# Performance work log

Hardware: AMD Instinct MI355X
Metric: run time of the kernel (lower is better)

Reference implementation:

```python
import jax, jax.numpy as jnp
import numpy as np


def _forward(x, wc, we, Wb1, bb1, Wb2, bb2, Wr1, br1, Wr2, br2,
             Wq1, bq1, Wq2, bq2, Wq3, bq3, Wo1, bo1, Wo2, bo2, Wo3, bo3, scale):
    bs, c, h, w = x.shape
    Hs, Ws = scale * h, scale * w
    fh = (jnp.arange(Hs, dtype=jnp.float32) + 0.5) / scale
    fw = (jnp.arange(Ws, dtype=jnp.float32) + 0.5) / scale
    coor_h = fh - jnp.floor(fh + 0.001) - 0.5  # [Hs] fractional phase
    coor_w = fw - jnp.floor(fw + 0.001) - 0.5  # [Ws]
    ones_hw = jnp.ones((Hs, Ws), jnp.float32)
    meta = jnp.stack([ones_hw, ones_hw / scale,
                      jnp.broadcast_to(coor_h[:, None], (Hs, Ws)),
                      jnp.broadcast_to(coor_w[None, :], (Hs, Ws))], 0)  # [4,Hs,Ws]
    chan_mean = x.mean(axis=(0, 2, 3))  # [c]
    chan_scale = jnp.concatenate([chan_mean[:, None], jnp.ones((c, 3), jnp.float32)], axis=1)  # [c,4]
    inp = meta[None] * chan_scale[:, :, None, None]  # [c,4,Hs,Ws]

    # body: 1x1x1 Conv3d over spectral-channel axis c
    lin = lambda W, b, t: jnp.einsum('oc,cfhw->ofhw', W, t) + b[:, None, None, None]
    emb = jax.nn.relu(lin(Wb2, bb2, jax.nn.relu(lin(Wb1, bb1, inp))))  # [c,4,Hs,Ws]

    # offset head: Conv2d 1x1 with batch = c, features = 4 -> 2
    lin2 = lambda W, b, t: jnp.einsum('of,cfhw->cohw', W, t) + b[None, :, None, None]
    off = lin2(Wo3, bo3, jax.nn.relu(lin2(Wo2, bo2, jax.nn.relu(lin2(Wo1, bo1, emb)))))  # [c,2,Hs,Ws]

    # routing_1: Conv3d over c -> 1 channel, sigmoid
    r = jax.nn.sigmoid(lin(Wr2, br2, jax.nn.relu(lin(Wr1, br1, emb))))[0]  # [4,Hs,Ws]
    # routing_2: Conv2d 1x1 over the 4 meta-features -> E experts
    lin3 = lambda W, b, t: jnp.einsum('of,fhw->ohw', W, t) + b[:, None, None]
    rw = jax.nn.sigmoid(lin3(Wq3, bq3, jax.nn.relu(lin3(Wq2, bq2, jax.nn.relu(lin3(Wq1, bq1, r))))))  # [E,Hs,Ws]

    # per-channel offset grid_sample (bilinear, zeros padding, align_corners=True)
    px0 = fw - 0.5  # [Ws] base source x coord
    py0 = fh - 0.5  # [Hs]

    def sample(img, offx, offy):  # img [bs,h,w]; off* [Hs,Ws]
        px = px0[None, :] + offx
        py = py0[:, None] + offy
        x0 = jnp.floor(px); y0 = jnp.floor(py)
        wx = px - x0; wy = py - y0
        x0i = x0.astype(jnp.int32); y0i = y0.astype(jnp.int32)
        def g(yi, xi):
            v = ((xi >= 0) & (xi <= w - 1) & (yi >= 0) & (yi <= h - 1)).astype(img.dtype)
            return img[:, jnp.clip(yi, 0, h - 1), jnp.clip(xi, 0, w - 1)] * v[None]
        return (g(y0i, x0i) * ((1 - wy) * (1 - wx))[None]
                + g(y0i, x0i + 1) * ((1 - wy) * wx)[None]
                + g(y0i + 1, x0i) * (wy * (1 - wx))[None]
                + g(y0i + 1, x0i + 1) * (wy * wx)[None])

    fea0 = jax.vmap(lambda xi, oi: sample(xi, oi[0], oi[1]),
                    in_axes=(1, 0), out_axes=1)(x, off)  # [bs,c,Hs,Ws]

    # per-pixel expert-mixed compress/expand: (sum_e r_e Wc_e) f then (sum_e r_e We_e)
    mid = jnp.einsum('ehw,ekc,bchw->bkhw', rw, wc, fea0)   # [bs,c//8,Hs,Ws]
    out = jnp.einsum('ehw,eck,bkhw->bchw', rw, we, mid)    # [bs,c,Hs,Ws]
    return out + fea0


def setup_inputs() -> dict:
    key = jax.random.key(0)
    ks = jax.random.split(key, 32)
    bs, c, h, w = 4, 64, 64, 64
    E, k = 4, c // 8
    s = 0.05
    d = {
        'x': jax.random.normal(ks[0], (bs, c, h, w), jnp.float32),
        'wc': jax.random.normal(ks[1], (E, k, c), jnp.float32) * s,
        'we': jax.random.normal(ks[2], (E, c, k), jnp.float32) * s,
        'Wb1': jax.random.normal(ks[3], (c, c), jnp.float32) * s,
        'bb1': jax.random.normal(ks[4], (c,), jnp.float32) * s,
        'Wb2': jax.random.normal(ks[5], (c, c), jnp.float32) * s,
        'bb2': jax.random.normal(ks[6], (c,), jnp.float32) * s,
        'Wr1': jax.random.normal(ks[7], (64, c), jnp.float32) * s,
        'br1': jax.random.normal(ks[8], (64,), jnp.float32) * s,
        'Wr2': jax.random.normal(ks[9], (1, 64), jnp.float32) * s,
        'br2': jax.random.normal(ks[10], (1,), jnp.float32) * s,
        'Wq1': jax.random.normal(ks[11], (64, 4), jnp.float32) * s,
        'bq1': jax.random.normal(ks[12], (64,), jnp.float32) * s,
        'Wq2': jax.random.normal(ks[13], (64, 64), jnp.float32) * s,
        'bq2': jax.random.normal(ks[14], (64,), jnp.float32) * s,
        'Wq3': jax.random.normal(ks[15], (E, 64), jnp.float32) * s,
        'bq3': jax.random.normal(ks[16], (E,), jnp.float32) * s,
        'Wo1': jax.random.normal(ks[17], (64, 4), jnp.float32) * s,
        'bo1': jax.random.normal(ks[18], (64,), jnp.float32) * s,
        'Wo2': jax.random.normal(ks[19], (64, 64), jnp.float32) * s,
        'bo2': jax.random.normal(ks[20], (64,), jnp.float32) * s,
        'Wo3': jax.random.normal(ks[21], (2, 64), jnp.float32) * s,
        'bo3': jax.random.normal(ks[22], (2,), jnp.float32) * s,
        'scale': 4,
    }
    return d


def reference(x, wc, we, Wb1, bb1, Wb2, bb2, Wr1, br1, Wr2, br2,
              Wq1, bq1, Wq2, bq2, Wq3, bq3, Wo1, bo1, Wo2, bo2, Wo3, bo3, scale):
    return _forward(x, wc, we, Wb1, bb1, Wb2, bb2, Wr1, br1, Wr2, br2,
                    Wq1, bq1, Wq2, bq2, Wq3, bq3, Wo1, bo1, Wo2, bo2, Wo3, bo3, int(scale))
```

## Files before the change

kernel.cpp:

```cpp
#include <hip/hip_runtime.h>


__device__ __forceinline__ float relu_(float v){ return fmaxf(v, 0.f); }
__device__ __forceinline__ float sigm_(float v){ return 1.f/(1.f + __expf(-v)); }

__global__ void k_mean(const float* __restrict__ x, float* __restrict__ ws) {
  const int ch = blockIdx.x, b = blockIdx.y, t = threadIdx.x;
  const float4* p = reinterpret_cast<const float4*>(x + (size_t)(b*64 + ch)*4096);
  float4 v0 = p[t], v1 = p[t+256], v2 = p[t+512], v3 = p[t+768];
  float s = ((v0.x+v0.y)+(v0.z+v0.w)) + ((v1.x+v1.y)+(v1.z+v1.w))
          + ((v2.x+v2.y)+(v2.z+v2.w)) + ((v3.x+v3.y)+(v3.z+v3.w));
  __shared__ float red[256];
  red[t] = s; __syncthreads();
  for (int off = 128; off > 0; off >>= 1) {
    if (t < off) red[t] += red[t + off];
    __syncthreads();
  }
  if (t == 0) ws[18496 + b*64 + ch] = red[0];
}

__launch_bounds__(256)
__global__ void k_phase(const float* __restrict__ wc, const float* __restrict__ we,
    const float* __restrict__ Wb1, const float* __restrict__ bb1,
    const float* __restrict__ Wb2, const float* __restrict__ bb2,
    const float* __restrict__ Wr1, const float* __restrict__ br1,
    const float* __restrict__ Wr2, const float* __restrict__ br2,
    const float* __restrict__ Wq1, const float* __restrict__ bq1,
    const float* __restrict__ Wq2, const float* __restrict__ bq2,
    const float* __restrict__ Wq3, const float* __restrict__ bq3,
    const float* __restrict__ Wo1, const float* __restrict__ bo1,
    const float* __restrict__ Wo2, const float* __restrict__ bo2,
    const float* __restrict__ Wo3, const float* __restrict__ bo3,
    float* __restrict__ ws)
{
  const int p = blockIdx.x, pi = p >> 2, pj = p & 3;
  const int t = threadIdx.x;
  const float chv = 0.25f*pi - 0.375f, cwv = 0.25f*pj - 0.375f;

  __shared__ float WbL1[64*66];
  __shared__ float WbL2[64*66];
  __shared__ float WrL1[64*66];
  __shared__ float WqL2[64*66];
  __shared__ __align__(16) float Wo2L[4096];
  __shared__ __align__(16) float Wo1L[256];
  __shared__ __align__(16) float wcL[2048];
  __shared__ __align__(16) float weL[2048];
  __shared__ float Wo3L[128];
  __shared__ float Wq1L[256], Wq3L[256];
  __shared__ float Wr2L[64];
  __shared__ float bb1L[64], bb2L[64], br1L[64], bq1L[64], bq2L[64];
  __shared__ float bo1L[64], bo2L[64];

  __shared__ float meanL[64];
  __shared__ __align__(16) float t1L[64][4];
  __shared__ __align__(16) float embL[64][4];
  __shared__ __align__(16) float rpL[64][4];
  __shared__ float r4[4];
  __shared__ float q1L[64], q2L[64];
  __shared__ float rwL[4];
  __shared__ float oxL[64][4], oyL[64][4];

  {
    const float* srcs[4] = {Wb1, Wb2, Wr1, Wq2};
    float* dsts[4] = {WbL1, WbL2, WrL1, WqL2};
    for (int m = 0; m < 4; ++m) {
      const float4* W4 = reinterpret_cast<const float4*>(srcs[m]);
      float* WL = dsts[m];
      for (int v = t; v < 1024; v += 256) {
        float4 d = W4[v];
        const int r = v >> 4, c = (v & 15) << 2;
        float* q = &WL[r*66 + c];
        q[0] = d.x; q[1] = d.y; q[2] = d.z; q[3] = d.w;
      }
    }
    for (int v = t; v < 1024; v += 256)
      reinterpret_cast<float4*>(Wo2L)[v] = reinterpret_cast<const float4*>(Wo2)[v];
    for (int v = t; v < 512; v += 256) {
      reinterpret_cast<float4*>(wcL)[v] = reinterpret_cast<const float4*>(wc)[v];
      reinterpret_cast<float4*>(weL)[v] = reinterpret_cast<const float4*>(we)[v];
    }
    if (t < 64) {
      reinterpret_cast<float4*>(Wo1L)[t] = reinterpret_cast<const float4*>(Wo1)[t];
      reinterpret_cast<float4*>(Wq1L)[t] = reinterpret_cast<const float4*>(Wq1)[t];
      reinterpret_cast<float4*>(Wq3L)[t] = reinterpret_cast<const float4*>(Wq3)[t];
      bb1L[t] = bb1[t]; bb2L[t] = bb2[t]; br1L[t] = br1[t];
      bq1L[t] = bq1[t]; bq2L[t] = bq2[t];
      bo1L[t] = bo1[t]; bo2L[t] = bo2[t];
      Wr2L[t] = Wr2[t];
      const float* wsp = ws + 18496;
      meanL[t] = (wsp[t] + wsp[64+t] + wsp[128+t] + wsp[192+t]) * (1.f/16384.f);
    }
    if (t >= 64 && t < 192) Wo3L[t-64] = Wo3[t-64];
  }
  __syncthreads();

  if (t < 64) {
    float a0 = 0.f, as = 0.f;
    const float* row = &WbL1[t*66];
    #pragma unroll 8
    for (int c = 0; c < 64; ++c) { float w = row[c]; a0 += w*meanL[c]; as += w; }
    float bb = bb1L[t];
    t1L[t][0] = relu_(a0 + bb);
    t1L[t][1] = relu_(0.25f*as + bb);
    t1L[t][2] = relu_(chv*as + bb);
    t1L[t][3] = relu_(cwv*as + bb);
  }
  __syncthreads();
  if (t < 64) {
    float bb = bb2L[t];
    float e0=bb,e1=bb,e2=bb,e3=bb;
    const float* row = &WbL2[t*66];
    #pragma unroll 8
    for (int c = 0; c < 64; ++c) {
      float w = row[c];
      float4 tv = *reinterpret_cast<const float4*>(&t1L[c][0]);
      e0 += w*tv.x; e1 += w*tv.y; e2 += w*tv.z; e3 += w*tv.w;
    }
    embL[t][0]=relu_(e0); embL[t][1]=relu_(e1); embL[t][2]=relu_(e2); embL[t][3]=relu_(e3);
  }
  __syncthreads();
  if (t < 64) {
    float bb = br1L[t];
    float p0=bb,p1=bb,p2=bb,p3=bb;
    const float* row = &WrL1[t*66];
    #pragma unroll 8
    for (int c = 0; c < 64; ++c) {
      float w = row[c];
      float4 ev = *reinterpret_cast<const float4*>(&embL[c][0]);
      p0 += w*ev.x; p1 += w*ev.y; p2 += w*ev.z; p3 += w*ev.w;
    }
    rpL[t][0]=relu_(p0); rpL[t][1]=relu_(p1); rpL[t][2]=relu_(p2); rpL[t][3]=relu_(p3);
  }
  __syncthreads();
  if (t < 4) {
    float acc = br2[0];
    #pragma unroll 8
    for (int c = 0; c < 64; ++c) acc += Wr2L[c]*rpL[c][t];
    r4[t] = sigm_(acc);
  }
  __syncthreads();
  if (t < 64) {
    float acc = bq1L[t];
    #pragma unroll
    for (int f = 0; f < 4; ++f) acc += Wq1L[t*4+f]*r4[f];
    q1L[t] = relu_(acc);
  }
  __syncthreads();
  if (t < 64) {
    float acc = bq2L[t];
    const float* row = &WqL2[t*66];
    #pragma unroll 8
    for (int c = 0; c < 64; ++c) acc += row[c]*q1L[c];
    q2L[t] = relu_(acc);
  }
  __syncthreads();
  if (t < 4) {
    float acc = bq3[t];
    #pragma unroll 8
    for (int c = 0; c < 64; ++c) acc += Wq3L[t*64+c]*q2L[c];
    rwL[t] = sigm_(acc);
  }
  __syncthreads();

  {
    const int ch = t & 63, q = t >> 6;
    const float4 e = *reinterpret_cast<const float4*>(&embL[ch][0]);
    float v1[64];
    #pragma unroll
    for (int o = 0; o < 64; ++o) {
      float4 w = *reinterpret_cast<const float4*>(&Wo1L[o*4]);
      v1[o] = relu_(w.x*e.x + w.y*e.y + w.z*e.z + w.w*e.w + bo1L[o]);
    }
    float ox = 0.f, oy = 0.f;
    for (int o = q*16; o < q*16+16; ++o) {
      float acc = bo2L[o];
      const float4* row = reinterpret_cast<const float4*>(&Wo2L[o*64]);
      #pragma unroll
      for (int k = 0; k < 16; ++k) {
        float4 w = row[k];
        acc += w.x*v1[4*k+0] + w.y*v1[4*k+1] + w.z*v1[4*k+2] + w.w*v1[4*k+3];
      }
      acc = relu_(acc);
      ox += Wo3L[o]*acc;
      oy += Wo3L[64+o]*acc;
    }
    oxL[ch][q] = ox; oyL[ch][q] = oy;
  }
  __syncthreads();

  float* ws_off = ws + 64;
  float* ws_wcT = ws + 2112;
  float* ws_weT = ws + 10304;
  if (t < 64) {
    ws_off[(p*64+t)*2+0] = oxL[t][0]+oxL[t][1]+oxL[t][2]+oxL[t][3] + bo3[0];
    ws_off[(p*64+t)*2+1] = oyL[t][0]+oyL[t][1]+oyL[t][2]+oyL[t][3] + bo3[1];
  }
  const float r0 = rwL[0], r1 = rwL[1], r2 = rwL[2], r3 = rwL[3];
  for (int idx = t; idx < 512; idx += 256) {
    const int ch = idx >> 3, k = idx & 7;
    ws_wcT[p*512 + idx] = r0*wcL[(0*8+k)*64+ch] + r1*wcL[(1*8+k)*64+ch]
                        + r2*wcL[(2*8+k)*64+ch] + r3*wcL[(3*8+k)*64+ch];
    ws_weT[p*512 + idx] = r0*weL[(0*64+ch)*8+k] + r1*weL[(1*64+ch)*8+k]
                        + r2*weL[(2*64+ch)*8+k] + r3*weL[(3*64+ch)*8+k];
  }
}

__launch_bounds__(256, 3)
__global__ void k_main(const float* __restrict__ x, const float* __restrict__ ws,
                       float* __restrict__ out) {
  const int i = blockIdx.x;
  const int b = blockIdx.y;
  const int j = threadIdx.x;
  const int pi = i & 3;
  const int pj = j & 3;

  __shared__ float wcT[4*520];
  __shared__ float weT[4*520];
  __shared__ float offxL[4*68];
  __shared__ int4  rowi[256];

  const float* wsoff = ws + 64;
  const float* wswc  = ws + 2112;
  const float* wswe  = ws + 10304;

  for (int idx = threadIdx.x; idx < 2048; idx += 256) {
    const int ph = idx >> 9, rem = idx & 511;
    wcT[ph*520 + rem] = wswc[(pi*4 + ph)*512 + rem];
    weT[ph*520 + rem] = wswe[(pi*4 + ph)*512 + rem];
  }
  {
    const int ch = threadIdx.x >> 2, ph = threadIdx.x & 3;
    const int p = pi*4 + ph;
    const float ox = wsoff[(p*64 + ch)*2 + 0];
    const float oy = wsoff[(p*64 + ch)*2 + 1];
    offxL[ph*68 + ch] = ox;
    const float py = i*0.25f - 0.375f + oy;
    const float fy = floorf(py);
    const float wy = py - fy;
    const int y0 = (int)fy, y1 = y0 + 1;
    const int y0c = min(max(y0, 0), 63), y1c = min(max(y1, 0), 63);
    const float wy0 = ((unsigned)y0 <= 63u) ? (1.f - wy) : 0.f;
    const float wy1 = ((unsigned)y1 <= 63u) ? wy : 0.f;
    rowi[ch*4 + ph] = make_int4(ch*4096 + y0c*64, ch*4096 + y1c*64,
                                __float_as_int(wy0), __float_as_int(wy1));
  }
  __syncthreads();

  const float* __restrict__ xb = x + (size_t)b*64*4096;
  const float px0 = j*0.25f - 0.375f;

  float fea[64];
  float mid[8] = {0.f,0.f,0.f,0.f,0.f,0.f,0.f,0.f};

  const float4* wc_pj = reinterpret_cast<const float4*>(&wcT[pj*520]);
  const float* offx_pj = &offxL[pj*68];
  const int4* rowi_pj = &rowi[pj];

  #pragma unroll
  for (int ch = 0; ch < 64; ++ch) {
    const int4 ri = rowi_pj[ch*4];
    const float px = px0 + offx_pj[ch];
    const float fx = floorf(px);
    const float wx = px - fx;
    const int x0 = (int)fx, x1 = x0 + 1;
    const int x0c = min(max(x0, 0), 63), x1c = min(max(x1, 0), 63);
    const float wx0 = ((unsigned)x0 <= 63u) ? (1.f - wx) : 0.f;
    const float wx1 = ((unsigned)x1 <= 63u) ? wx : 0.f;
    const float g00 = xb[ri.x + x0c], g01 = xb[ri.x + x1c];
    const float g10 = xb[ri.y + x0c], g11 = xb[ri.y + x1c];
    const float f0 = g00*wx0 + g01*wx1;
    const float f1 = g10*wx0 + g11*wx1;
    const float fv = f0*__int_as_float(ri.z) + f1*__int_as_float(ri.w);
    fea[ch] = fv;
    const float4 wa = wc_pj[ch*2], wb = wc_pj[ch*2+1];
    mid[0] += wa.x*fv; mid[1] += wa.y*fv; mid[2] += wa.z*fv; mid[3] += wa.w*fv;
    mid[4] += wb.x*fv; mid[5] += wb.y*fv; mid[6] += wb.z*fv; mid[7] += wb.w*fv;
  }

  const float4* we_pj = reinterpret_cast<const float4*>(&weT[pj*520]);
  float* op = out + (size_t)(b*64)*65536 + i*256 + j;
  #pragma unroll
  for (int ch = 0; ch < 64; ++ch) {
    const float4 wa = we_pj[ch*2], wb = we_pj[ch*2+1];
    float acc = fea[ch];
    acc += wa.x*mid[0] + wa.y*mid[1] + wa.z*mid[2] + wa.w*mid[3];
    acc += wb.x*mid[4] + wb.y*mid[5] + wb.z*mid[6] + wb.w*mid[7];
    op[ch*65536] = acc;
  }
}

extern "C" void kernel_launch(void* const* d_in, const int* in_sizes, int n_in,
                              void* d_out, int out_size, void* d_ws, size_t ws_size,
                              hipStream_t stream) {
  const float* x   = (const float*)d_in[0];
  const float* wc  = (const float*)d_in[1];
  const float* we  = (const float*)d_in[2];
  const float* Wb1 = (const float*)d_in[3];
  const float* bb1 = (const float*)d_in[4];
  const float* Wb2 = (const float*)d_in[5];
  const float* bb2 = (const float*)d_in[6];
  const float* Wr1 = (const float*)d_in[7];
  const float* br1 = (const float*)d_in[8];
  const float* Wr2 = (const float*)d_in[9];
  const float* br2 = (const float*)d_in[10];
  const float* Wq1 = (const float*)d_in[11];
  const float* bq1 = (const float*)d_in[12];
  const float* Wq2 = (const float*)d_in[13];
  const float* bq2 = (const float*)d_in[14];
  const float* Wq3 = (const float*)d_in[15];
  const float* bq3 = (const float*)d_in[16];
  const float* Wo1 = (const float*)d_in[17];
  const float* bo1 = (const float*)d_in[18];
  const float* Wo2 = (const float*)d_in[19];
  const float* bo2 = (const float*)d_in[20];
  const float* Wo3 = (const float*)d_in[21];
  const float* bo3 = (const float*)d_in[22];
  float* ws  = (float*)d_ws;
  float* out = (float*)d_out;

  k_mean<<<dim3(64, 4), 256, 0, stream>>>(x, ws);
  k_phase<<<16, 256, 0, stream>>>(wc, we, Wb1, bb1, Wb2, bb2, Wr1, br1, Wr2, br2,
                                  Wq1, bq1, Wq2, bq2, Wq3, bq3,
                                  Wo1, bo1, Wo2, bo2, Wo3, bo3, ws);
  k_main<<<dim3(256, 4), 256, 0, stream>>>(x, ws, out);
}
```

Before: 160.8 us.

## Split channel loop across two thread halves with shared-memory mid reduction

k_main now launches 512 threads per block, and each half handles 32 of the 64 channels. Partial 8-wide mid accumulators are exchanged through shared memory and summed before the expansion stage. Per-channel x-phase floor and weights are precomputed once into shared memory, and byte offsets replace index arithmetic. The aim is more wavefront parallelism and fewer live registers (fea[32] instead of fea[64]), at the cost of an extra barrier and shared-memory traffic.

```diff
diff --git a/kernel.cpp b/kernel.cpp
--- a/kernel.cpp
+++ b/kernel.cpp
@@ -205,35 +205,37 @@
   }
 }
 
-__launch_bounds__(256, 3)
+__launch_bounds__(512, 6)
 __global__ void k_main(const float* __restrict__ x, const float* __restrict__ ws,
                        float* __restrict__ out) {
   const int i = blockIdx.x;
   const int b = blockIdx.y;
-  const int j = threadIdx.x;
+  const int t = threadIdx.x;
+  const int j = t & 255;
+  const int h = t >> 8;
+  const int pj = j & 3, jb = j >> 2;
   const int pi = i & 3;
-  const int pj = j & 3;
 
   __shared__ float wcT[4*520];
   __shared__ float weT[4*520];
-  __shared__ float offxL[4*68];
-  __shared__ int4  rowi[256];
+  __shared__ int4  gA[256];
+  __shared__ int4  gB[256];
+  __shared__ float midL[2*8*256];
 
   const float* wsoff = ws + 64;
   const float* wswc  = ws + 2112;
   const float* wswe  = ws + 10304;
 
-  for (int idx = threadIdx.x; idx < 2048; idx += 256) {
+  for (int idx = t; idx < 2048; idx += 512) {
     const int ph = idx >> 9, rem = idx & 511;
     wcT[ph*520 + rem] = wswc[(pi*4 + ph)*512 + rem];
     weT[ph*520 + rem] = wswe[(pi*4 + ph)*512 + rem];
   }
-  {
-    const int ch = threadIdx.x >> 2, ph = threadIdx.x & 3;
+  if (t < 256) {
+    const int ch = t >> 2, ph = t & 3;
     const int p = pi*4 + ph;
     const float ox = wsoff[(p*64 + ch)*2 + 0];
     const float oy = wsoff[(p*64 + ch)*2 + 1];
-    offxL[ph*68 + ch] = ox;
     const float py = i*0.25f - 0.375f + oy;
     const float fy = floorf(py);
     const float wy = py - fy;
@@ -241,51 +243,64 @@
     const int y0c = min(max(y0, 0), 63), y1c = min(max(y1, 0), 63);
     const float wy0 = ((unsigned)y0 <= 63u) ? (1.f - wy) : 0.f;
     const float wy1 = ((unsigned)y1 <= 63u) ? wy : 0.f;
-    rowi[ch*4 + ph] = make_int4(ch*4096 + y0c*64, ch*4096 + y1c*64,
-                                __float_as_int(wy0), __float_as_int(wy1));
-  }
-  __syncthreads();
-
-  const float* __restrict__ xb = x + (size_t)b*64*4096;
-  const float px0 = j*0.25f - 0.375f;
-
-  float fea[64];
+    gA[ch*4 + ph] = make_int4((ch*4096 + y0c*64)*4, (ch*4096 + y1c*64)*4,
+                              __float_as_int(wy0), __float_as_int(wy1));
+    const float tx = ph*0.25f - 0.375f + ox;
+    const float ftx = floorf(tx);
+    const float wx = tx - ftx;
+    gB[ch*4 + ph] = make_int4((int)ftx, __float_as_int(1.f - wx),
+                              __float_as_int(wx), 0);
+  }
+  __syncthreads();
+
+  const char* __restrict__ xbc = (const char*)(x + (size_t)b*64*4096);
+
+  float fea[32];
   float mid[8] = {0.f,0.f,0.f,0.f,0.f,0.f,0.f,0.f};
 
-  const float4* wc_pj = reinterpret_cast<const float4*>(&wcT[pj*520]);
-  const float* offx_pj = &offxL[pj*68];
-  const int4* rowi_pj = &rowi[pj];
+  const float4* wc_pj = reinterpret_cast<const float4*>(&wcT[pj*520 + h*256]);
+  const int4* gA_p = &gA[h*128 + pj];
+  const int4* gB_p = &gB[h*128 + pj];
 
   #pragma unroll
-  for (int ch = 0; ch < 64; ++ch) {
-    const int4 ri = rowi_pj[ch*4];
-    const float px = px0 + offx_pj[ch];
-    const float fx = floorf(px);
-    const float wx = px - fx;
-    const int x0 = (int)fx, x1 = x0 + 1;
-    const int x0c = min(max(x0, 0), 63), x1c = min(max(x1, 0), 63);
-    const float wx0 = ((unsigned)x0 <= 63u) ? (1.f - wx) : 0.f;
-    const float wx1 = ((unsigned)x1 <= 63u) ? wx : 0.f;
-    const float g00 = xb[ri.x + x0c], g01 = xb[ri.x + x1c];
-    const float g10 = xb[ri.y + x0c], g11 = xb[ri.y + x1c];
+  for (int k = 0; k < 32; ++k) {
+    const int4 ra = gA_p[k*4];
+    const int4 rb = gB_p[k*4];
+    const int x0 = jb + rb.x;
+    const int x1 = x0 + 1;
+    const int x0c = min(max(x0, 0), 63);
+    const int x1c = min(max(x1, 0), 63);
+    const float wx0 = ((unsigned)x0 <= 63u) ? __int_as_float(rb.y) : 0.f;
+    const float wx1 = ((unsigned)x1 <= 63u) ? __int_as_float(rb.z) : 0.f;
+    const float g00 = *(const float*)(xbc + ra.x + (x0c << 2));
+    const float g01 = *(const float*)(xbc + ra.x + (x1c << 2));
+    const float g10 = *(const float*)(xbc + ra.y + (x0c << 2));
+    const float g11 = *(const float*)(xbc + ra.y + (x1c << 2));
     const float f0 = g00*wx0 + g01*wx1;
     const float f1 = g10*wx0 + g11*wx1;
-    const float fv = f0*__int_as_float(ri.z) + f1*__int_as_float(ri.w);
-    fea[ch] = fv;
-    const float4 wa = wc_pj[ch*2], wb = wc_pj[ch*2+1];
+    const float fv = f0*__int_as_float(ra.z) + f1*__int_as_float(ra.w);
+    fea[k] = fv;
+    const float4 wa = wc_pj[k*2], wb = wc_pj[k*2+1];
     mid[0] += wa.x*fv; mid[1] += wa.y*fv; mid[2] += wa.z*fv; mid[3] += wa.w*fv;
     mid[4] += wb.x*fv; mid[5] += wb.y*fv; mid[6] += wb.z*fv; mid[7] += wb.w*fv;
   }
 
-  const float4* we_pj = reinterpret_cast<const float4*>(&weT[pj*520]);
-  float* op = out + (size_t)(b*64)*65536 + i*256 + j;
   #pragma unroll
-  for (int ch = 0; ch < 64; ++ch) {
-    const float4 wa = we_pj[ch*2], wb = we_pj[ch*2+1];
-    float acc = fea[ch];
+  for (int m = 0; m < 8; ++m) midL[(h*8 + m)*256 + j] = mid[m];
+  __syncthreads();
+  const int oh = 1 - h;
+  #pragma unroll
+  for (int m = 0; m < 8; ++m) mid[m] += midL[(oh*8 + m)*256 + j];
+
+  const float4* we_pj = reinterpret_cast<const float4*>(&weT[pj*520 + h*256]);
+  float* op = out + (size_t)b*64*65536 + (size_t)(h*32)*65536 + i*256 + j;
+  #pragma unroll
+  for (int k = 0; k < 32; ++k) {
+    const float4 wa = we_pj[k*2], wb = we_pj[k*2+1];
+    float acc = fea[k];
     acc += wa.x*mid[0] + wa.y*mid[1] + wa.z*mid[2] + wa.w*mid[3];
     acc += wb.x*mid[4] + wb.y*mid[5] + wb.z*mid[6] + wb.w*mid[7];
-    op[ch*65536] = acc;
+    op[k*65536] = acc;
   }
 }
 
@@ -322,5 +337,5 @@
   k_phase<<<16, 256, 0, stream>>>(wc, we, Wb1, bb1, Wb2, bb2, Wr1, br1, Wr2, br2,
                                   Wq1, bq1, Wq2, bq2, Wq3, bq3,
                                   Wo1, bo1, Wo2, bo2, Wo3, bo3, ws);
-  k_main<<<dim3(256, 4), 256, 0, stream>>>(x, ws, out);
+  k_main<<<dim3(256, 4), 512, 0, stream>>>(x, ws, out);
 }
```

Result: no change. 160.9 us (+0.0%).
